# Optimization experiments

Hardware: AMD Instinct MI355X
Metric: run time of the kernel (lower is better)

Reference implementation:

```python
import jax, jax.numpy as jnp
import numpy as np

B, V, T, C, HIN, WIN = 1, 6, 3, 256, 32, 32
NH = 8
LN_EPS = 1e-5


def setup_inputs() -> dict:
    key = jax.random.key(0)
    ks = jax.random.split(key, 14)
    s = 0.02
    lim = 1.0 / np.sqrt(C)
    def lin_w(k):
        return jax.random.uniform(k, (C, C), jnp.float32, -lim, lim)
    return {
        "history_feats": jax.random.normal(ks[0], (B, V, T, C, HIN, WIN), jnp.float32),
        "query_embed": jax.random.normal(ks[1], (1, C, 1, 1), jnp.float32) * s,
        "camera_pos_embed": jax.random.normal(ks[2], (V, C), jnp.float32) * s,
        "temporal_pos_embed": jax.random.normal(ks[3], (T, C), jnp.float32) * s,
        "spatial_pos_embed": jax.random.normal(ks[4], (1, C, 1, 1), jnp.float32) * s,
        "q_w": lin_w(ks[5]), "q_b": jnp.zeros((C,), jnp.float32),
        "k_w": lin_w(ks[6]), "k_b": jnp.zeros((C,), jnp.float32),
        "v_w": lin_w(ks[7]), "v_b": jnp.zeros((C,), jnp.float32),
        "o_w": lin_w(ks[8]), "o_b": jnp.zeros((C,), jnp.float32),
        "ln_g": jnp.ones((C,), jnp.float32),
        "ln_b": jnp.zeros((C,), jnp.float32),
        "query_cam_idx": 0,
        "H": 32,
        "W": 32,
    }


def reference(history_feats, query_embed, camera_pos_embed, temporal_pos_embed,
              spatial_pos_embed, q_w, q_b, k_w, k_b, v_w, v_b, o_w, o_b,
              ln_g, ln_b, query_cam_idx, H, W):
    B_, V_, T_, C_, Hin, Win = history_feats.shape
    dh = C_ // NH
    # --- build query: [B, H*W, C] ---
    q = query_embed + camera_pos_embed[query_cam_idx][None, :, None, None] + spatial_pos_embed
    q = jnp.broadcast_to(q, (B_, C_, H, W)).reshape(B_, C_, H * W).transpose(0, 2, 1)
    kv = (history_feats
          + temporal_pos_embed[None, None, :, :, None, None]
          + camera_pos_embed[None, :, None, :, None, None])
    kv = kv.transpose(0, 1, 2, 4, 5, 3).reshape(B_, V_ * T_ * Hin * Win, C_)
    # --- projections (torch Linear: x @ W.T + b) ---
    qp = q @ q_w.T + q_b
    kp = kv @ k_w.T + k_b
    vp = kv @ v_w.T + v_b
    # --- split heads: [B, NH, L, dh] ---
    qh = qp.reshape(B_, H * W, NH, dh).transpose(0, 2, 1, 3)
    kh = kp.reshape(B_, -1, NH, dh).transpose(0, 2, 1, 3)
    vh = vp.reshape(B_, -1, NH, dh).transpose(0, 2, 1, 3)
    scale = float(dh) ** -0.5
    attn = jax.nn.softmax(jnp.einsum('bhqd,bhkd->bhqk', qh, kh) * scale, axis=-1)
    out = jnp.einsum('bhqk,bhkd->bhqd', attn, vh)
    out = out.transpose(0, 2, 1, 3).reshape(B_, H * W, C_)
    out = out @ o_w.T + o_b
    # --- LayerNorm over channel dim ---
    mu = out.mean(-1, keepdims=True)
    var = ((out - mu) ** 2).mean(-1, keepdims=True)
    out = (out - mu) * jax.lax.rsqrt(var + LN_EPS) * ln_g + ln_b
    return out.transpose(0, 2, 1).reshape(B_, C_, H, W)
```

## Files before the change

### kernel.cpp

```cpp
#include <hip/hip_runtime.h>
#include <hip/hip_fp16.h>

typedef const float* fcp;

#define C_    256
#define NH_   8
#define DH_   32
#define VT_   18
#define HWK   1024
#define L_    (VT_*HWK)
#define SCALE_ 0.17677669529663687f

#define EMB_OFF  0
#define WF_OFF   4608
#define BB_OFF   6656
#define PSVT_OFF 6720
#define Y_OFF    6912
#define Z_OFF    7168
#define CTXP_OFF 7424

__device__ __forceinline__ float blockReduceSum256(float v){
  __shared__ float red[4];
  #pragma unroll
  for (int off = 32; off; off >>= 1) v += __shfl_xor(v, off, 64);
  const int lane = threadIdx.x & 63, w = threadIdx.x >> 6;
  __syncthreads();
  if (lane == 0) red[w] = v;
  __syncthreads();
  return red[0] + red[1] + red[2] + red[3];
}

__global__ void k_fold(fcp qe, fcp cam, fcp tpe, fcp spe, const int* __restrict__ cidx,
                       fcp qw, fcp qb, fcp kw, fcp kb, float* __restrict__ ws){
  __shared__ float qvS[C_];
  __shared__ float qpS[DH_];
  const int b = blockIdx.x, t = threadIdx.x, lane = t & 63, wv = t >> 6;
  const int ci = cidx[0];
  qvS[t] = qe[t] + cam[ci*C_ + t] + spe[t];
  {
    const int v = b/3, tt = b - v*3;
    ws[EMB_OFF + b*C_ + t] = tpe[tt*C_ + t] + cam[v*C_ + t];
  }
  {
    #pragma unroll
    for (int i = 0; i < 8; i++) ws[CTXP_OFF + b*2048 + i*256 + t] = 0.f;
    if (b == 8 && t < 144) ws[PSVT_OFF + t] = 0.f;
  }
  __syncthreads();
  if (b < 8){
    #pragma unroll
    for (int i = 0; i < 8; i++){
      const int r = b*DH_ + wv*8 + i;
      fcp qr = qw + (size_t)r*C_;
      float v = qr[lane]*qvS[lane] + qr[64+lane]*qvS[64+lane]
              + qr[128+lane]*qvS[128+lane] + qr[192+lane]*qvS[192+lane];
      #pragma unroll
      for (int off = 32; off; off >>= 1) v += __shfl_xor(v, off, 64);
      if (lane == 0) qpS[wv*8 + i] = v + qb[r];
    }
    __syncthreads();
    float acc = 0.f;
    #pragma unroll 8
    for (int d = 0; d < DH_; d++)
      acc += qpS[d] * kw[(size_t)(b*DH_ + d)*C_ + t];
    ws[WF_OFF + b*C_ + t] = SCALE_ * acc;
    if (t == 0){
      float bb = 0.f;
      for (int d = 0; d < DH_; d++) bb += qpS[d] * kb[b*DH_ + d];
      ws[BB_OFF + b] = SCALE_ * bb;
    }
  }
}

__global__ void k_attn(fcp feats, float* __restrict__ ws){
  __shared__ __align__(16) float wf[C_*8];
  __shared__ float redS[32];
  __shared__ float basef[8];
  __shared__ float predS[512];
  __shared__ float pexS[64*8];
  __shared__ __align__(16) __half fS[8*32*66];
  const int bid = blockIdx.x, vt = bid >> 4, sc = bid & 15, t = threadIdx.x;

  predS[t] = 0.f;
  for (int idx = t; idx < 2048; idx += 512){
    const int h = idx >> 8, c = idx & 255;
    wf[c*8 + h] = ws[WF_OFF + idx];
  }
  __syncthreads();
  if (t < 256){
    const float e = ws[EMB_OFF + vt*C_ + t];
    const float4 wa = *(const float4*)&wf[t*8];
    const float4 wb = *(const float4*)&wf[t*8 + 4];
    float pb[8] = {e*wa.x, e*wa.y, e*wa.z, e*wa.w, e*wb.x, e*wb.y, e*wb.z, e*wb.w};
    #pragma unroll
    for (int h = 0; h < 8; h++){
      float v = pb[h];
      #pragma unroll
      for (int off = 32; off; off >>= 1) v += __shfl_xor(v, off, 64);
      if ((t & 63) == 0) redS[(t >> 6)*8 + h] = v;
    }
  }
  __syncthreads();
  if (t < 8) basef[t] = redS[t] + redS[8+t] + redS[16+t] + redS[24+t] + ws[BB_OFF + t];
  __syncthreads();
  const int s = t & 63, cg = t >> 6;
  fcp fp = feats + ((size_t)vt*C_ + cg*32)*HWK + sc*64 + s;
  float fv[32];
  #pragma unroll
  for (int i = 0; i < 32; i++) fv[i] = fp[(size_t)i*HWK];
  float acc[8] = {0,0,0,0,0,0,0,0};
  #pragma unroll
  for (int i = 0; i < 32; i++){
    fS[(cg*32 + i)*66 + s] = __float2half(fv[i]);
    const float4 wa = *(const float4*)&wf[(cg*32+i)*8];
    const float4 wb = *(const float4*)&wf[(cg*32+i)*8 + 4];
    acc[0] += fv[i]*wa.x; acc[1] += fv[i]*wa.y; acc[2] += fv[i]*wa.z; acc[3] += fv[i]*wa.w;
    acc[4] += fv[i]*wb.x; acc[5] += fv[i]*wb.y; acc[6] += fv[i]*wb.z; acc[7] += fv[i]*wb.w;
  }
  #pragma unroll
  for (int h = 0; h < 8; h++)
    atomicAdd(&predS[h*64 + s], acc[h]);
  __syncthreads();
  {
    const int h1 = t >> 6, tok = t & 63;
    const float sum = basef[h1] + predS[t];
    const float e = __expf(sum);
    pexS[tok*8 + h1] = e;
    float v = e;
    #pragma unroll
    for (int off = 32; off; off >>= 1) v += __shfl_xor(v, off, 64);
    if (tok == 0) atomicAdd(&ws[PSVT_OFF + vt*8 + h1], v);
  }
  __syncthreads();
  const int lane = t & 63, hB = lane & 7, isub = lane >> 3;
  float aB[4] = {0.f, 0.f, 0.f, 0.f};
  #pragma unroll 4
  for (int s2 = 0; s2 < 64; s2 += 2){
    const float pe0 = pexS[s2*8 + hB];
    const float pe1 = pexS[s2*8 + 8 + hB];
    #pragma unroll
    for (int p = 0; p < 4; p++){
      const __half2 h2 = *(const __half2*)&fS[(cg*32 + p*8 + isub)*66 + s2];
      const float2 f2 = __half22float2(h2);
      aB[p] += pe0 * f2.x + pe1 * f2.y;
    }
  }
  #pragma unroll
  for (int p = 0; p < 4; p++)
    atomicAdd(&ws[CTXP_OFF + vt*2048 + hB*256 + cg*32 + p*8 + isub], aB[p]);
}

__global__ void k_vproj(fcp vw, fcp vb, float* __restrict__ ws){
  __shared__ float psS[144];
  const int r = blockIdx.x, t = threadIdx.x, h = r >> 5;
  if (t < 144) psS[t] = ws[PSVT_OFF + t];
  __syncthreads();
  float denom = 0.f, embP = 0.f, ctx = 0.f;
  #pragma unroll
  for (int vt = 0; vt < VT_; vt++){
    const float P = psS[vt*8 + h];
    denom += P;
    embP  += ws[EMB_OFF + vt*C_ + t] * P;
    ctx   += ws[CTXP_OFF + vt*2048 + h*256 + t];
  }
  const float ctxn = (ctx + embP) / denom;
  float v = vw[(size_t)r*C_ + t] * ctxn;
  v = blockReduceSum256(v);
  if (t == 0) ws[Y_OFF + r] = v + vb[r];
}

__global__ void k_oproj(fcp ow, fcp ob, float* __restrict__ ws){
  const int r = blockIdx.x, t = threadIdx.x;
  float v = ow[(size_t)r*C_ + t] * ws[Y_OFF + t];
  v = blockReduceSum256(v);
  if (t == 0) ws[Z_OFF + r] = v + ob[r];
}

__global__ void k_out(fcp lng, fcp lnb, const float* __restrict__ ws,
                      float* __restrict__ out, int hw){
  const int c = blockIdx.x, t = threadIdx.x;
  const float z = ws[Z_OFF + t];
  const float s  = blockReduceSum256(z);
  const float s2 = blockReduceSum256(z*z);
  const float mu = s * (1.f/C_);
  const float var = s2 * (1.f/C_) - mu*mu;
  const float rs = rsqrtf(var + 1e-5f);
  const float fin = (ws[Z_OFF + c] - mu) * rs * lng[c] + lnb[c];
  float4 pk = make_float4(fin, fin, fin, fin);
  ((float4*)(out + (size_t)c*hw))[t] = pk;
}

extern "C" void kernel_launch(void* const* d_in, const int* in_sizes, int n_in,
                              void* d_out, int out_size, void* d_ws, size_t ws_size,
                              hipStream_t stream) {
  fcp feats = (fcp)d_in[0];
  fcp qe    = (fcp)d_in[1];
  fcp cam   = (fcp)d_in[2];
  fcp tpe   = (fcp)d_in[3];
  fcp spe   = (fcp)d_in[4];
  fcp qw    = (fcp)d_in[5];
  fcp qb    = (fcp)d_in[6];
  fcp kw    = (fcp)d_in[7];
  fcp kb    = (fcp)d_in[8];
  fcp vw    = (fcp)d_in[9];
  fcp vb    = (fcp)d_in[10];
  fcp ow    = (fcp)d_in[11];
  fcp ob    = (fcp)d_in[12];
  fcp lng   = (fcp)d_in[13];
  fcp lnb   = (fcp)d_in[14];
  const int* cidx = (const int*)d_in[15];
  float* ws = (float*)d_ws;
  float* out = (float*)d_out;
  const int hw = out_size / C_;

  k_fold  <<<18,  256, 0, stream>>>(qe, cam, tpe, spe, cidx, qw, qb, kw, kb, ws);
  k_attn  <<<288, 512, 0, stream>>>(feats, ws);
  k_vproj <<<256, 256, 0, stream>>>(vw, vb, ws);
  k_oproj <<<256, 256, 0, stream>>>(ow, ob, ws);
  k_out   <<<256, 256, 0, stream>>>(lng, lnb, ws, out, hw);
}
```

Baseline: 134.5 us.

## Fuse v-proj, o-proj and LayerNorm into attention kernel via grid barriers

```diff
diff --git a/kernel.cpp b/kernel.cpp
--- a/kernel.cpp
+++ b/kernel.cpp
@@ -18,17 +18,7 @@
 #define Y_OFF    6912
 #define Z_OFF    7168
 #define CTXP_OFF 7424
-
-__device__ __forceinline__ float blockReduceSum256(float v){
-  __shared__ float red[4];
-  #pragma unroll
-  for (int off = 32; off; off >>= 1) v += __shfl_xor(v, off, 64);
-  const int lane = threadIdx.x & 63, w = threadIdx.x >> 6;
-  __syncthreads();
-  if (lane == 0) red[w] = v;
-  __syncthreads();
-  return red[0] + red[1] + red[2] + red[3];
-}
+#define BAR_OFF  44288
 
 __global__ void k_fold(fcp qe, fcp cam, fcp tpe, fcp spe, const int* __restrict__ cidx,
                        fcp qw, fcp qb, fcp kw, fcp kb, float* __restrict__ ws){
@@ -45,6 +35,7 @@
     #pragma unroll
     for (int i = 0; i < 8; i++) ws[CTXP_OFF + b*2048 + i*256 + t] = 0.f;
     if (b == 8 && t < 144) ws[PSVT_OFF + t] = 0.f;
+    if (b == 9 && t < 3)   ((unsigned*)(ws + BAR_OFF))[t] = 0u;
   }
   __syncthreads();
   if (b < 8){
@@ -72,7 +63,8 @@
   }
 }
 
-__global__ void k_attn(fcp feats, float* __restrict__ ws){
+__global__ void k_attn(fcp feats, fcp vw, fcp vb, fcp ow, fcp ob, fcp lng, fcp lnb,
+                       float* __restrict__ ws, float* __restrict__ out, int hw){
   __shared__ __align__(16) float wf[C_*8];
   __shared__ float redS[32];
   __shared__ float basef[8];
@@ -80,6 +72,7 @@
   __shared__ float pexS[64*8];
   __shared__ __align__(16) __half fS[8*32*66];
   const int bid = blockIdx.x, vt = bid >> 4, sc = bid & 15, t = threadIdx.x;
+  unsigned* bars = (unsigned*)(ws + BAR_OFF);
 
   predS[t] = 0.f;
   for (int idx = t; idx < 2048; idx += 512){
@@ -105,17 +98,21 @@
   __syncthreads();
   const int s = t & 63, cg = t >> 6;
   fcp fp = feats + ((size_t)vt*C_ + cg*32)*HWK + sc*64 + s;
-  float fv[32];
-  #pragma unroll
-  for (int i = 0; i < 32; i++) fv[i] = fp[(size_t)i*HWK];
   float acc[8] = {0,0,0,0,0,0,0,0};
   #pragma unroll
-  for (int i = 0; i < 32; i++){
-    fS[(cg*32 + i)*66 + s] = __float2half(fv[i]);
-    const float4 wa = *(const float4*)&wf[(cg*32+i)*8];
-    const float4 wb = *(const float4*)&wf[(cg*32+i)*8 + 4];
-    acc[0] += fv[i]*wa.x; acc[1] += fv[i]*wa.y; acc[2] += fv[i]*wa.z; acc[3] += fv[i]*wa.w;
-    acc[4] += fv[i]*wb.x; acc[5] += fv[i]*wb.y; acc[6] += fv[i]*wb.z; acc[7] += fv[i]*wb.w;
+  for (int half = 0; half < 2; half++){
+    float fv[16];
+    #pragma unroll
+    for (int i = 0; i < 16; i++) fv[i] = fp[(size_t)(half*16 + i)*HWK];
+    #pragma unroll
+    for (int i = 0; i < 16; i++){
+      const int ch = half*16 + i;
+      fS[(cg*32 + ch)*66 + s] = __float2half(fv[i]);
+      const float4 wa = *(const float4*)&wf[(cg*32+ch)*8];
+      const float4 wb = *(const float4*)&wf[(cg*32+ch)*8 + 4];
+      acc[0] += fv[i]*wa.x; acc[1] += fv[i]*wa.y; acc[2] += fv[i]*wa.z; acc[3] += fv[i]*wa.w;
+      acc[4] += fv[i]*wb.x; acc[5] += fv[i]*wb.y; acc[6] += fv[i]*wb.z; acc[7] += fv[i]*wb.w;
+    }
   }
   #pragma unroll
   for (int h = 0; h < 8; h++)
@@ -148,46 +145,101 @@
   #pragma unroll
   for (int p = 0; p < 4; p++)
     atomicAdd(&ws[CTXP_OFF + vt*2048 + hB*256 + cg*32 + p*8 + isub], aB[p]);
-}
-
-__global__ void k_vproj(fcp vw, fcp vb, float* __restrict__ ws){
-  __shared__ float psS[144];
-  const int r = blockIdx.x, t = threadIdx.x, h = r >> 5;
-  if (t < 144) psS[t] = ws[PSVT_OFF + t];
-  __syncthreads();
-  float denom = 0.f, embP = 0.f, ctx = 0.f;
-  #pragma unroll
-  for (int vt = 0; vt < VT_; vt++){
-    const float P = psS[vt*8 + h];
-    denom += P;
-    embP  += ws[EMB_OFF + vt*C_ + t] * P;
-    ctx   += ws[CTXP_OFF + vt*2048 + h*256 + t];
-  }
-  const float ctxn = (ctx + embP) / denom;
-  float v = vw[(size_t)r*C_ + t] * ctxn;
-  v = blockReduceSum256(v);
-  if (t == 0) ws[Y_OFF + r] = v + vb[r];
-}
-
-__global__ void k_oproj(fcp ow, fcp ob, float* __restrict__ ws){
-  const int r = blockIdx.x, t = threadIdx.x;
-  float v = ow[(size_t)r*C_ + t] * ws[Y_OFF + t];
-  v = blockReduceSum256(v);
-  if (t == 0) ws[Z_OFF + r] = v + ob[r];
-}
-
-__global__ void k_out(fcp lng, fcp lnb, const float* __restrict__ ws,
-                      float* __restrict__ out, int hw){
-  const int c = blockIdx.x, t = threadIdx.x;
-  const float z = ws[Z_OFF + t];
-  const float s  = blockReduceSum256(z);
-  const float s2 = blockReduceSum256(z*z);
-  const float mu = s * (1.f/C_);
+
+  __threadfence();
+  __syncthreads();
+  if (t == 0){
+    __hip_atomic_fetch_add(&bars[0], 1u, __ATOMIC_ACQ_REL, __HIP_MEMORY_SCOPE_AGENT);
+    while (__hip_atomic_load(&bars[0], __ATOMIC_ACQUIRE, __HIP_MEMORY_SCOPE_AGENT) < 288u)
+      __builtin_amdgcn_s_sleep(1);
+  }
+  __syncthreads();
+  if (bid >= 256) return;
+
+  float* psS  = predS;
+  float* red8 = predS + 160;
+  float* red8b= predS + 176;
+  if (t < 144)
+    psS[t] = __hip_atomic_load(&ws[PSVT_OFF + t], __ATOMIC_RELAXED, __HIP_MEMORY_SCOPE_AGENT);
+  __syncthreads();
+  const int r = bid, hR = r >> 5;
+  float v1 = 0.f;
+  if (t < 256){
+    float denom = 0.f, embP = 0.f, ctx = 0.f;
+    #pragma unroll
+    for (int v2 = 0; v2 < VT_; v2++){
+      const float P = psS[v2*8 + hR];
+      denom += P;
+      embP  += ws[EMB_OFF + v2*C_ + t] * P;
+      ctx   += __hip_atomic_load(&ws[CTXP_OFF + v2*2048 + hR*256 + t],
+                                 __ATOMIC_RELAXED, __HIP_MEMORY_SCOPE_AGENT);
+    }
+    v1 = vw[(size_t)r*C_ + t] * ((ctx + embP) / denom);
+  }
+  #pragma unroll
+  for (int off = 32; off; off >>= 1) v1 += __shfl_xor(v1, off, 64);
+  if ((t & 63) == 0) red8[t >> 6] = v1;
+  __syncthreads();
+  if (t == 0){
+    float sy = vb[r];
+    #pragma unroll
+    for (int i = 0; i < 8; i++) sy += red8[i];
+    __hip_atomic_store(&ws[Y_OFF + r], sy, __ATOMIC_RELAXED, __HIP_MEMORY_SCOPE_AGENT);
+  }
+  __threadfence();
+  __syncthreads();
+  if (t == 0){
+    __hip_atomic_fetch_add(&bars[1], 1u, __ATOMIC_ACQ_REL, __HIP_MEMORY_SCOPE_AGENT);
+    while (__hip_atomic_load(&bars[1], __ATOMIC_ACQUIRE, __HIP_MEMORY_SCOPE_AGENT) < 256u)
+      __builtin_amdgcn_s_sleep(1);
+  }
+  __syncthreads();
+
+  float v2 = 0.f;
+  if (t < 256)
+    v2 = ow[(size_t)r*C_ + t] *
+         __hip_atomic_load(&ws[Y_OFF + t], __ATOMIC_RELAXED, __HIP_MEMORY_SCOPE_AGENT);
+  #pragma unroll
+  for (int off = 32; off; off >>= 1) v2 += __shfl_xor(v2, off, 64);
+  if ((t & 63) == 0) red8[t >> 6] = v2;
+  __syncthreads();
+  if (t == 0){
+    float sz = ob[r];
+    #pragma unroll
+    for (int i = 0; i < 8; i++) sz += red8[i];
+    __hip_atomic_store(&ws[Z_OFF + r], sz, __ATOMIC_RELAXED, __HIP_MEMORY_SCOPE_AGENT);
+  }
+  __threadfence();
+  __syncthreads();
+  if (t == 0){
+    __hip_atomic_fetch_add(&bars[2], 1u, __ATOMIC_ACQ_REL, __HIP_MEMORY_SCOPE_AGENT);
+    while (__hip_atomic_load(&bars[2], __ATOMIC_ACQUIRE, __HIP_MEMORY_SCOPE_AGENT) < 256u)
+      __builtin_amdgcn_s_sleep(1);
+  }
+  __syncthreads();
+
+  float* zS = pexS;
+  if (t < 256)
+    zS[t] = __hip_atomic_load(&ws[Z_OFF + t], __ATOMIC_RELAXED, __HIP_MEMORY_SCOPE_AGENT);
+  __syncthreads();
+  const float zv = (t < 256) ? zS[t] : 0.f;
+  float a1 = zv, a2 = zv*zv;
+  #pragma unroll
+  for (int off = 32; off; off >>= 1){
+    a1 += __shfl_xor(a1, off, 64);
+    a2 += __shfl_xor(a2, off, 64);
+  }
+  if ((t & 63) == 0){ red8[t >> 6] = a1; red8b[t >> 6] = a2; }
+  __syncthreads();
+  float s1 = 0.f, s2 = 0.f;
+  #pragma unroll
+  for (int i = 0; i < 8; i++){ s1 += red8[i]; s2 += red8b[i]; }
+  const float mu = s1 * (1.f/C_);
   const float var = s2 * (1.f/C_) - mu*mu;
   const float rs = rsqrtf(var + 1e-5f);
-  const float fin = (ws[Z_OFF + c] - mu) * rs * lng[c] + lnb[c];
-  float4 pk = make_float4(fin, fin, fin, fin);
-  ((float4*)(out + (size_t)c*hw))[t] = pk;
+  const float fin = (zS[r] - mu) * rs * lng[r] + lnb[r];
+  if (t < 256)
+    ((float4*)(out + (size_t)r*hw))[t] = make_float4(fin, fin, fin, fin);
 }
 
 extern "C" void kernel_launch(void* const* d_in, const int* in_sizes, int n_in,
@@ -213,9 +265,6 @@
   float* out = (float*)d_out;
   const int hw = out_size / C_;
 
-  k_fold  <<<18,  256, 0, stream>>>(qe, cam, tpe, spe, cidx, qw, qb, kw, kb, ws);
-  k_attn  <<<288, 512, 0, stream>>>(feats, ws);
-  k_vproj <<<256, 256, 0, stream>>>(vw, vb, ws);
-  k_oproj <<<256, 256, 0, stream>>>(ow, ob, ws);
-  k_out   <<<256, 256, 0, stream>>>(lng, lnb, ws, out, hw);
+  k_fold <<<18,  256, 0, stream>>>(qe, cam, tpe, spe, cidx, qw, qb, kw, kb, ws);
+  k_attn <<<288, 512, 0, stream>>>(feats, vw, vb, ow, ob, lng, lnb, ws, out, hw);
 }
```

New measurement: 281.4 us. 109% more time.
